# Performance work log

Measured on AMD Instinct MI355X. Metric: run time of the kernel, lower is better.

Reference implementation:

```python
import jax, jax.numpy as jnp
import numpy as np

N, E = 100000, 1600000
F_IN, H, HG, L, C = 128, 128, 128, 3, 40


def setup_inputs() -> dict:
    key = jax.random.key(0)
    ks = jax.random.split(key, 12)
    s = 0.05
    return dict(
        x=jax.random.normal(ks[0], (N, F_IN), jnp.float32),
        edge_index=jax.random.randint(ks[1], (2, E), 0, N),
        edge_weight=jax.random.uniform(ks[2], (E,), jnp.float32),
        h0=jax.random.normal(ks[3], (N, HG), jnp.float32),
        linW=jax.random.normal(ks[4], (F_IN, H), jnp.float32) * s,
        linB=jnp.zeros((H,), jnp.float32),
        convW=jax.random.normal(ks[5], (L, H, H), jnp.float32) * s,
        convB=jnp.zeros((L, H), jnp.float32),
        gru_Wih=jax.random.normal(ks[6], (3 * HG, H), jnp.float32) * s,
        gru_Whh=jax.random.normal(ks[7], (3 * HG, HG), jnp.float32) * s,
        gru_bih=jnp.zeros((3 * HG,), jnp.float32),
        gru_bhh=jnp.zeros((3 * HG,), jnp.float32),
        fcW=jax.random.normal(ks[8], (HG, C), jnp.float32) * s,
        fcB=jnp.zeros((C,), jnp.float32),
    )


def _gru(x, h, Wih, Whh, bih, bhh):
    # torch.nn.GRUCell math (gate order: r, z, n)
    gi = x @ Wih.T + bih  # [N, 3*HG]
    gh = h @ Whh.T + bhh  # [N, 3*HG]
    ir, iz, in_ = jnp.split(gi, 3, axis=-1)
    hr, hz, hn = jnp.split(gh, 3, axis=-1)
    r = jax.nn.sigmoid(ir + hr)
    z = jax.nn.sigmoid(iz + hz)
    n = jnp.tanh(in_ + r * hn)
    return (1.0 - z) * n + z * h


def _gcn_conv(x, src, dst, ew, W, b, n_nodes):
    # PyG GCNConv: linear -> symmetric-normalized sparse aggregation -> bias
    xw = x @ W  # [N, H]
    deg = jax.ops.segment_sum(ew, dst, num_segments=n_nodes)
    dinv = jnp.where(deg > 0, jax.lax.rsqrt(deg), 0.0)
    norm = dinv[src] * ew * dinv[dst]  # [E+N]
    msg = xw[src] * norm[:, None]      # gather + scale (irregular access)
    out = jax.ops.segment_sum(msg, dst, num_segments=n_nodes)  # scatter-add
    return out + b


def reference(x, edge_index, edge_weight, h0, linW, linB, convW, convB,
              gru_Wih, gru_Whh, gru_bih, gru_bhh, fcW, fcB):
    n_nodes = x.shape[0]
    # GCNConv default: add self-loops with weight 1 before normalization
    loops = jnp.arange(n_nodes)
    src = jnp.concatenate([edge_index[0], loops])
    dst = jnp.concatenate([edge_index[1], loops])
    ew = jnp.concatenate([edge_weight, jnp.ones((n_nodes,), edge_weight.dtype)])

    h = h0
    xh = jax.nn.relu(x @ linW + linB)
    h = _gru(xh, h, gru_Wih, gru_Whh, gru_bih, gru_bhh)
    for l in range(convW.shape[0]):  # fixed small layer count
        xh = jax.nn.relu(_gcn_conv(xh, src, dst, ew, convW[l], convB[l], n_nodes))
        h = _gru(xh, h, gru_Wih, gru_Whh, gru_bih, gru_bhh)
    return h @ fcW + fcB
```

## Files before the change

### kernel.cpp

```cpp
#include <hip/hip_runtime.h>
#include <hip/hip_bf16.h>
#include <math.h>

typedef __attribute__((ext_vector_type(8))) short bf8_t;
typedef __attribute__((ext_vector_type(4))) float f4_t;
typedef __attribute__((ext_vector_type(8))) unsigned short us8_t;

__device__ inline unsigned short f2bf(float f) {
  union { float f; unsigned u; } x; x.f = f;
  unsigned r = x.u + 0x7FFF + ((x.u >> 16) & 1);
  return (unsigned short)(r >> 16);
}
__device__ inline float bflo(unsigned v) {
  union { unsigned u; float f; } x; x.u = v << 16; return x.f;
}
__device__ inline float bfhi(unsigned v) {
  union { unsigned u; float f; } x; x.u = v & 0xFFFF0000u; return x.f;
}
__device__ inline float fast_sig(float x) {
  return __builtin_amdgcn_rcpf(1.f + __expf(-x));
}
__device__ inline float fast_tanh(float x) {
  return 1.f - 2.f * __builtin_amdgcn_rcpf(1.f + __expf(2.f * x));
}

__device__ inline void async_copy16(const void* g, void* l) {
  __builtin_amdgcn_global_load_lds(
      (const __attribute__((address_space(1))) unsigned int*)g,
      (__attribute__((address_space(3))) unsigned int*)l, 16, 0, 0);
}

__device__ inline bf8_t pack_bf8(const float* p) {
  float4 a = *(const float4*)p;
  float4 b = *(const float4*)(p + 4);
  bf8_t t;
  t[0] = (short)f2bf(a.x); t[1] = (short)f2bf(a.y);
  t[2] = (short)f2bf(a.z); t[3] = (short)f2bf(a.w);
  t[4] = (short)f2bf(b.x); t[5] = (short)f2bf(b.y);
  t[6] = (short)f2bf(b.z); t[7] = (short)f2bf(b.w);
  return t;
}


__device__ inline void packB_body(const float* __restrict__ W,
                                  unsigned short* __restrict__ out,
                                  int K, int Ncols, int ldw, int trans, int bid) {
  int idx = bid * 256 + threadIdx.x;
  int total = (Ncols / 16) * (K / 32) * 64;
  if (idx >= total) return;
  int lane = idx & 63;
  int frag = idx >> 6;
  int kt = K / 32;
  int k0 = frag % kt;
  int n0 = frag / kt;
  int n = n0 * 16 + (lane & 15);
  int kbase = k0 * 32 + (lane >> 4) * 8;
  us8_t v;
#pragma unroll
  for (int j = 0; j < 8; ++j) {
    int k = kbase + j;
    float f = trans ? W[(size_t)n * ldw + k] : W[(size_t)k * ldw + n];
    v[j] = f2bf(f);
  }
  *(us8_t*)(out + (size_t)idx * 8) = v;
}

template<bool RELU, bool BIAS, bool F32A>
__device__ inline void gemm_body4(const void* __restrict__ Araw,
                                  const unsigned short* __restrict__ Bp,
                                  const float* __restrict__ bias,
                                  unsigned short* __restrict__ C, int M, int bid,
                                  unsigned char* smem) {
  int wave = threadIdx.x >> 6, lane = threadIdx.x & 63;
  int row0 = (bid * 4 + wave) * 16;
  int m = lane & 15, q = lane >> 4;

#pragma unroll
  for (int i = 0; i < 8; ++i) {
    int f = wave * 8 + i;
    async_copy16((const unsigned char*)Bp + (size_t)f * 1024 + lane * 16,
                 smem + f * 1024);
  }
  __syncthreads();
  if (row0 >= M) return;

  int arow = row0 + m; if (arow >= M) arow = M - 1;
  bf8_t a[4];
#pragma unroll
  for (int k0 = 0; k0 < 4; ++k0) {
    if (F32A) {
      a[k0] = pack_bf8((const float*)Araw + (size_t)arow * 128 + k0 * 32 + q * 8);
    } else {
      a[k0] = *(const bf8_t*)((const unsigned short*)Araw +
                              (size_t)arow * 128 + k0 * 32 + q * 8);
    }
  }

#pragma unroll
  for (int n0 = 0; n0 < 8; ++n0) {
    f4_t acc = {};
#pragma unroll
    for (int k0 = 0; k0 < 4; ++k0) {
      bf8_t b = *(const bf8_t*)(smem + (n0 * 4 + k0) * 1024 + lane * 16);
      acc = __builtin_amdgcn_mfma_f32_16x16x32_bf16(a[k0], b, acc, 0, 0, 0);
    }
    int col = n0 * 16 + m;
    float bs = BIAS ? bias[col] : 0.f;
#pragma unroll
    for (int r = 0; r < 4; ++r) {
      int grow = row0 + q * 4 + r;
      if (grow < M) {
        float v = acc[r] + bs;
        if (RELU) v = fmaxf(v, 0.f);
        C[(size_t)grow * 128 + col] = f2bf(v);
      }
    }
  }
}

__device__ inline void gru_stage4(const unsigned short* __restrict__ Bi,
                                  const unsigned short* __restrict__ Bh,
                                  unsigned char* half, int wave, int lane, int g) {
#pragma unroll
  for (int s = 0; s < 6; ++s) {
    int cc = g + 8 * (s >= 3 ? s - 3 : s);
    const unsigned short* src = (s < 3) ? Bi : Bh;
    int f = s * 4 + wave;
    async_copy16((const unsigned char*)src + ((size_t)(cc * 4 + wave)) * 1024 + lane * 16,
                 half + f * 1024);
  }
}

__device__ inline void gru_core4(const bf8_t* ax, const float* h_in, float* h_out,
                                 const unsigned short* __restrict__ Bi,
                                 const unsigned short* __restrict__ Bh,
                                 const float* __restrict__ bih, const float* __restrict__ bhh,
                                 int M, int row0, int wave, int lane,
                                 unsigned char* smem) {
  int m = lane & 15, q = lane >> 4;
  int arow = row0 + m; if (arow >= M) arow = M - 1;

  bf8_t ah[4];
#pragma unroll
  for (int k0 = 0; k0 < 4; ++k0)
    ah[k0] = pack_bf8(h_in + (size_t)arow * 128 + k0 * 32 + q * 8);

  int erow[4];
#pragma unroll
  for (int r = 0; r < 4; ++r) {
    int gr = row0 + q * 4 + r;
    erow[r] = (gr < M) ? gr : (M - 1);
  }

  float hp_cur[4], hp_nxt[4];
#pragma unroll
  for (int r = 0; r < 4; ++r)
    hp_cur[r] = h_in[(size_t)erow[r] * 128 + m];

#pragma unroll
  for (int g = 0; g < 8; ++g) {
    __syncthreads();
    if (g < 7)
      gru_stage4(Bi, Bh, smem + ((g + 1) & 1) * (24 * 1024), wave, lane, g + 1);
    unsigned char* cur = smem + (g & 1) * (24 * 1024);

    f4_t air = {}, aiz = {}, ain = {}, ahr = {}, ahz = {}, ahn = {};
#pragma unroll
    for (int k0 = 0; k0 < 4; ++k0) {
      bf8_t br = *(const bf8_t*)(cur + (0 * 4 + k0) * 1024 + lane * 16);
      bf8_t bz = *(const bf8_t*)(cur + (1 * 4 + k0) * 1024 + lane * 16);
      bf8_t bn = *(const bf8_t*)(cur + (2 * 4 + k0) * 1024 + lane * 16);
      bf8_t cr = *(const bf8_t*)(cur + (3 * 4 + k0) * 1024 + lane * 16);
      bf8_t cz = *(const bf8_t*)(cur + (4 * 4 + k0) * 1024 + lane * 16);
      bf8_t cn = *(const bf8_t*)(cur + (5 * 4 + k0) * 1024 + lane * 16);
      air = __builtin_amdgcn_mfma_f32_16x16x32_bf16(ax[k0], br, air, 0, 0, 0);
      aiz = __builtin_amdgcn_mfma_f32_16x16x32_bf16(ax[k0], bz, aiz, 0, 0, 0);
      ain = __builtin_amdgcn_mfma_f32_16x16x32_bf16(ax[k0], bn, ain, 0, 0, 0);
      ahr = __builtin_amdgcn_mfma_f32_16x16x32_bf16(ah[k0], cr, ahr, 0, 0, 0);
      ahz = __builtin_amdgcn_mfma_f32_16x16x32_bf16(ah[k0], cz, ahz, 0, 0, 0);
      ahn = __builtin_amdgcn_mfma_f32_16x16x32_bf16(ah[k0], cn, ahn, 0, 0, 0);
    }
    if (g < 7) {
#pragma unroll
      for (int r = 0; r < 4; ++r)
        hp_nxt[r] = h_in[(size_t)erow[r] * 128 + (g + 1) * 16 + m];
    }

    int col = g * 16 + m;
    float bir_ = bih[col], biz_ = bih[col + 128], bin_ = bih[col + 256];
    float bhr_ = bhh[col], bhz_ = bhh[col + 128], bhn_ = bhh[col + 256];
#pragma unroll
    for (int r = 0; r < 4; ++r) {
      int grow = row0 + q * 4 + r;
      if (grow < M) {
        float rr = fast_sig(air[r] + bir_ + ahr[r] + bhr_);
        float zz = fast_sig(aiz[r] + biz_ + ahz[r] + bhz_);
        float nn = fast_tanh(ain[r] + bin_ + rr * (ahn[r] + bhn_));
        h_out[(size_t)grow * 128 + col] = (1.f - zz) * nn + zz * hp_cur[r];
      }
    }
#pragma unroll
    for (int r = 0; r < 4; ++r) hp_cur[r] = hp_nxt[r];
  }
}


__global__ __launch_bounds__(256) void k_prep(
    const float* __restrict__ linW, const float* __restrict__ convW,
    const float* __restrict__ Wih, const float* __restrict__ Whh,
    unsigned short* __restrict__ linWp, unsigned short* __restrict__ convWp,
    unsigned short* __restrict__ Bi, unsigned short* __restrict__ Bh,
    int* __restrict__ cnt, int N) {
  int b = blockIdx.x;
  if (b < 8)  { packB_body(linW, linWp, 128, 128, 128, 0, b); return; }
  if (b < 32) { int l = (b - 8) >> 3;
                packB_body(convW + (size_t)l * 16384, convWp + (size_t)l * 16384,
                           128, 128, 128, 0, (b - 8) & 7); return; }
  if (b < 56) { packB_body(Wih, Bi, 128, 384, 128, 1, b - 32); return; }
  if (b < 80) { packB_body(Whh, Bh, 128, 384, 128, 1, b - 56); return; }
  int i = (b - 80) * 256 + threadIdx.x;
  if (i < N) cnt[i] = 0;
}

__global__ __launch_bounds__(256) void k_count_lin(
    const int* __restrict__ dst, int* __restrict__ cnt, int* __restrict__ pos, int E,
    const float* __restrict__ x, const unsigned short* __restrict__ linWp,
    const float* __restrict__ linB, unsigned short* __restrict__ xh, int M,
    int nCnt) {
  __shared__ unsigned char smem[32 * 1024];
  if ((int)blockIdx.x < nCnt) {
    int e = blockIdx.x * 256 + threadIdx.x;
    if (e < E) pos[e] = atomicAdd(&cnt[dst[e]], 1);
    return;
  }
  gemm_body4<true, true, true>(x, linWp, linB, xh, M, blockIdx.x - nCnt, smem);
}

__global__ __launch_bounds__(256) void k_scan_block(
    const int* __restrict__ cnt, int* __restrict__ partial,
    int* __restrict__ bsum, int n) {
  __shared__ int s[256];
  int tid = threadIdx.x;
  int i = blockIdx.x * 256 + tid;
  s[tid] = (i < n) ? cnt[i] : 0;
  __syncthreads();
#pragma unroll
  for (int d = 1; d < 256; d <<= 1) {
    int t = (tid >= d) ? s[tid - d] : 0;
    __syncthreads();
    s[tid] += t;
    __syncthreads();
  }
  if (i < n) partial[i] = s[tid];
  if (tid == 255) bsum[blockIdx.x] = s[255];
}

__global__ __launch_bounds__(512) void k_scan_sums(int* __restrict__ bsum, int nb) {
  __shared__ int s[512];
  int tid = threadIdx.x;
  s[tid] = (tid < nb) ? bsum[tid] : 0;
  __syncthreads();
#pragma unroll
  for (int d = 1; d < 512; d <<= 1) {
    int t = (tid >= d) ? s[tid - d] : 0;
    __syncthreads();
    s[tid] += t;
    __syncthreads();
  }
  if (tid < nb) bsum[tid] = s[tid];
}

__global__ __launch_bounds__(256) void k_scan_add(
    const int* __restrict__ partial, const int* __restrict__ bsum,
    int* __restrict__ rowptr, int n) {
  int i = blockIdx.x * 256 + threadIdx.x;
  if (i == 0) rowptr[0] = 0;
  if (i < n) {
    int v = partial[i] + (blockIdx.x > 0 ? bsum[blockIdx.x - 1] : 0);
    rowptr[i + 1] = v;
  }
}

__global__ __launch_bounds__(512) void k_fill(
    const int* __restrict__ src, const int* __restrict__ dst,
    const float* __restrict__ ew, const int* __restrict__ rowptr,
    const int* __restrict__ pos, int2* __restrict__ csr, int E) {
  int e = blockIdx.x * 512 + threadIdx.x;
  if (e >= E) return;
  int d = dst[e];
  int p = rowptr[d] + pos[e];
  unsigned long long v = (unsigned long long)(unsigned)src[e] |
                         ((unsigned long long)(unsigned)__float_as_int(ew[e]) << 32);
  __builtin_nontemporal_store(v, (unsigned long long*)(csr + p));
}

__global__ __launch_bounds__(512) void k_deg(
    const int* __restrict__ rowptr, const int2* __restrict__ csr,
    float* __restrict__ dinv, int N) {
  int n = blockIdx.x * 512 + threadIdx.x;
  if (n >= N) return;
  int b = rowptr[n], e = rowptr[n + 1];
  float s = 1.0f;
  for (int j = b; j < e; ++j) {
    unsigned long long v = __builtin_nontemporal_load((const unsigned long long*)(csr + j));
    s += __int_as_float((int)(v >> 32));
  }
  dinv[n] = rsqrtf(s);
}

__global__ __launch_bounds__(512) void k_norm(
    const int* __restrict__ rowptr, int2* __restrict__ csr,
    const float* __restrict__ dinv, int N) {
  int n = blockIdx.x * 512 + threadIdx.x;
  if (n >= N) return;
  int b = rowptr[n], e = rowptr[n + 1];
  float dn = dinv[n];
  for (int j = b; j < e; ++j) {
    unsigned long long v = __builtin_nontemporal_load((const unsigned long long*)(csr + j));
    int s = (int)v;
    float w = dinv[s] * __int_as_float((int)(v >> 32)) * dn;
    unsigned long long nv = (unsigned long long)(unsigned)s |
                            ((unsigned long long)(unsigned)__float_as_int(w) << 32);
    __builtin_nontemporal_store(nv, (unsigned long long*)(csr + j));
  }
}

__global__ __launch_bounds__(256) void k_conv(
    const unsigned short* __restrict__ A, const unsigned short* __restrict__ Bp,
    unsigned short* __restrict__ C, int M) {
  __shared__ unsigned char smem[32 * 1024];
  gemm_body4<false, false, false>(A, Bp, nullptr, C, M, blockIdx.x, smem);
}

__global__ __launch_bounds__(256, 3) void k_gru(
    const unsigned short* __restrict__ xh, const float* h_in, float* h_out,
    const unsigned short* __restrict__ Bi, const unsigned short* __restrict__ Bh,
    const float* __restrict__ bih, const float* __restrict__ bhh, int M) {
  __shared__ unsigned char smem[2 * 24 * 1024];
  int wave = threadIdx.x >> 6, lane = threadIdx.x & 63;
  int row0 = (blockIdx.x * 4 + wave) * 16;
  gru_stage4(Bi, Bh, smem, wave, lane, 0);
  int m = lane & 15, q = lane >> 4;
  int arow = row0 + m; if (arow >= M) arow = M - 1;
  bf8_t ax[4];
#pragma unroll
  for (int k0 = 0; k0 < 4; ++k0)
    ax[k0] = *(const bf8_t*)(xh + (size_t)arow * 128 + k0 * 32 + q * 8);
  gru_core4(ax, h_in, h_out, Bi, Bh, bih, bhh, M, row0, wave, lane, smem);
}


__global__ __launch_bounds__(256) void k_gather(
    const int* __restrict__ rowptr, const int2* __restrict__ csr,
    const unsigned* __restrict__ xw,
    const float* __restrict__ dinv, const float* __restrict__ bias,
    unsigned* __restrict__ out, int N) {
  int wave = threadIdx.x >> 6;
  int lane = threadIdx.x & 63;
  int node = __builtin_amdgcn_readfirstlane(blockIdx.x * 4 + wave);
  if (node >= N) return;
  int beg = __builtin_amdgcn_readfirstlane(rowptr[node]);
  int end = __builtin_amdgcn_readfirstlane(rowptr[node + 1]);

  float accl = 0.f, acch = 0.f;
  int k = beg;
  for (; k + 4 <= end; k += 4) {
    unsigned long long r0 = __builtin_nontemporal_load((const unsigned long long*)(csr + k));
    unsigned long long r1 = __builtin_nontemporal_load((const unsigned long long*)(csr + k + 1));
    unsigned long long r2 = __builtin_nontemporal_load((const unsigned long long*)(csr + k + 2));
    unsigned long long r3 = __builtin_nontemporal_load((const unsigned long long*)(csr + k + 3));
    unsigned v0 = xw[((size_t)(unsigned)r0 << 6) + lane];
    unsigned v1 = xw[((size_t)(unsigned)r1 << 6) + lane];
    unsigned v2 = xw[((size_t)(unsigned)r2 << 6) + lane];
    unsigned v3 = xw[((size_t)(unsigned)r3 << 6) + lane];
    float w0 = __int_as_float((int)(r0 >> 32)), w1 = __int_as_float((int)(r1 >> 32));
    float w2 = __int_as_float((int)(r2 >> 32)), w3 = __int_as_float((int)(r3 >> 32));
    accl += bflo(v0) * w0; acch += bfhi(v0) * w0;
    accl += bflo(v1) * w1; acch += bfhi(v1) * w1;
    accl += bflo(v2) * w2; acch += bfhi(v2) * w2;
    accl += bflo(v3) * w3; acch += bfhi(v3) * w3;
  }
  for (; k < end; ++k) {
    unsigned long long r = __builtin_nontemporal_load((const unsigned long long*)(csr + k));
    unsigned v = xw[((size_t)(unsigned)r << 6) + lane];
    float w = __int_as_float((int)(r >> 32));
    accl += bflo(v) * w; acch += bfhi(v) * w;
  }

  float di = dinv[node];
  float sn = di * di;
  unsigned vs = xw[((size_t)node << 6) + lane];
  float2 b = *(const float2*)(bias + lane * 2);
  float rl = fmaxf(accl + bflo(vs) * sn + b.x, 0.f);
  float rh = fmaxf(acch + bfhi(vs) * sn + b.y, 0.f);
  unsigned o = (unsigned)f2bf(rl) | ((unsigned)f2bf(rh) << 16);
  out[((size_t)node << 6) + lane] = o;
}


template<bool RELU, bool BIAS>
__global__ __launch_bounds__(256) void k_gemm128(
    const float* __restrict__ A, const float* __restrict__ B,
    const float* __restrict__ bias, float* __restrict__ C, int M, int Nc) {
  __shared__ float As[64][36];
  __shared__ float Bs[32][64];
  int tid = threadIdx.x;
  int tx = tid & 15, ty = tid >> 4;
  int row0 = blockIdx.y * 64, col0 = blockIdx.x * 64;
  float acc[4][4] = {};

  for (int k0 = 0; k0 < 128; k0 += 32) {
#pragma unroll
    for (int i = 0; i < 2; ++i) {
      int f = tid + i * 256;
      int r = f >> 3, c4 = f & 7;
      int gr = row0 + r;
      float4 v = make_float4(0.f, 0.f, 0.f, 0.f);
      if (gr < M) v = *(const float4*)(A + (size_t)gr * 128 + k0 + c4 * 4);
      *(float4*)(&As[r][c4 * 4]) = v;
    }
#pragma unroll
    for (int i = 0; i < 2; ++i) {
      int f = tid + i * 256;
      int r = f >> 4, c4 = f & 15;
      int gc = col0 + c4 * 4;
      float4 v = make_float4(0.f, 0.f, 0.f, 0.f);
      if (gc + 3 < Nc) v = *(const float4*)(B + (size_t)(k0 + r) * Nc + gc);
      *(float4*)(&Bs[r][c4 * 4]) = v;
    }
    __syncthreads();
#pragma unroll
    for (int kk = 0; kk < 32; ++kk) {
      float4 b = *(float4*)(&Bs[kk][tx * 4]);
      float a0 = As[ty * 4 + 0][kk];
      float a1 = As[ty * 4 + 1][kk];
      float a2 = As[ty * 4 + 2][kk];
      float a3 = As[ty * 4 + 3][kk];
      acc[0][0] += a0 * b.x; acc[0][1] += a0 * b.y; acc[0][2] += a0 * b.z; acc[0][3] += a0 * b.w;
      acc[1][0] += a1 * b.x; acc[1][1] += a1 * b.y; acc[1][2] += a1 * b.z; acc[1][3] += a1 * b.w;
      acc[2][0] += a2 * b.x; acc[2][1] += a2 * b.y; acc[2][2] += a2 * b.z; acc[2][3] += a2 * b.w;
      acc[3][0] += a3 * b.x; acc[3][1] += a3 * b.y; acc[3][2] += a3 * b.z; acc[3][3] += a3 * b.w;
    }
    __syncthreads();
  }

#pragma unroll
  for (int i = 0; i < 4; ++i) {
    int gr = row0 + ty * 4 + i;
    if (gr >= M) continue;
#pragma unroll
    for (int j = 0; j < 4; ++j) {
      int gc = col0 + tx * 4 + j;
      if (gc >= Nc) continue;
      float v = acc[i][j];
      if (BIAS) v += bias[gc];
      if (RELU) v = fmaxf(v, 0.f);
      C[(size_t)gr * Nc + gc] = v;
    }
  }
}


extern "C" void kernel_launch(void* const* d_in, const int* in_sizes, int n_in,
                              void* d_out, int out_size, void* d_ws, size_t ws_size,
                              hipStream_t stream) {
  const float* x    = (const float*)d_in[0];
  const int*   ei   = (const int*)d_in[1];
  const float* ew   = (const float*)d_in[2];
  const float* h0   = (const float*)d_in[3];
  const float* linW = (const float*)d_in[4];
  const float* linB = (const float*)d_in[5];
  const float* convW= (const float*)d_in[6];
  const float* convB= (const float*)d_in[7];
  const float* Wih  = (const float*)d_in[8];
  const float* Whh  = (const float*)d_in[9];
  const float* bih  = (const float*)d_in[10];
  const float* bhh  = (const float*)d_in[11];
  const float* fcW  = (const float*)d_in[12];
  const float* fcB  = (const float*)d_in[13];

  int N = in_sizes[0] / 128;
  int E = in_sizes[1] / 2;
  const int* srcI = ei;
  const int* dstI = ei + E;
  int nb = (N + 255) / 256;

  float* ws = (float*)d_ws;
  size_t off = 0;
  float* dinv = ws + off; off += (size_t)N;
  if (off & 1) off++;
  float* h    = ws + off; off += (size_t)N * 128;
  int* iws = (int*)(ws + off);
  size_t ioff = 0;
  int2* csr    = (int2*)iws; ioff += (size_t)2 * E;
  int* cnt     = iws + ioff; ioff += (size_t)N;
  int* partial = iws + ioff; ioff += (size_t)N;
  int* bsum    = iws + ioff; ioff += 512;
  int* rowptr  = iws + ioff; ioff += (size_t)N + 1;
  ioff = (ioff + 3) & ~(size_t)3;
  unsigned short* usws = (unsigned short*)(iws + ioff);
  size_t uoff = 0;
  unsigned short* xh_bf  = usws + uoff; uoff += (size_t)N * 128;
  unsigned short* xw_bf  = usws + uoff; uoff += (size_t)N * 128;
  unsigned short* linWp  = usws + uoff; uoff += 128 * 128;
  unsigned short* convWp = usws + uoff; uoff += 3 * 128 * 128;
  unsigned short* Bi     = usws + uoff; uoff += 384 * 128;
  unsigned short* Bh     = usws + uoff; uoff += 384 * 128;

  int* pos = (int*)xw_bf;

  int gw4  = (N + 63) / 64;
  int nCnt = (E + 255) / 256;
  int n512 = (N + 511) / 512;
  int e512 = (E + 511) / 512;
  int ggat = (N + 3) / 4;

  k_prep<<<80 + nb, 256, 0, stream>>>(linW, convW, Wih, Whh,
                                      linWp, convWp, Bi, Bh, cnt, N);
  k_count_lin<<<nCnt + gw4, 256, 0, stream>>>(dstI, cnt, pos, E,
                                              x, linWp, linB, xh_bf, N, nCnt);
  k_scan_block<<<nb, 256, 0, stream>>>(cnt, partial, bsum, N);
  k_scan_sums<<<1, 512, 0, stream>>>(bsum, nb);
  k_scan_add<<<nb, 256, 0, stream>>>(partial, bsum, rowptr, N);
  k_fill<<<e512, 512, 0, stream>>>(srcI, dstI, ew, rowptr, pos, csr, E);
  k_deg<<<n512, 512, 0, stream>>>(rowptr, csr, dinv, N);
  k_norm<<<n512, 512, 0, stream>>>(rowptr, csr, dinv, N);
  k_gru<<<gw4, 256, 0, stream>>>(xh_bf, h0, h, Bi, Bh, bih, bhh, N);
  for (int l = 0; l < 3; ++l) {
    k_conv<<<gw4, 256, 0, stream>>>(
        xh_bf, convWp + (size_t)l * 128 * 128, xw_bf, N);
    k_gather<<<ggat, 256, 0, stream>>>(
        rowptr, csr, (const unsigned*)xw_bf, dinv, convB + (size_t)l * 128,
        (unsigned*)xh_bf, N);
    k_gru<<<gw4, 256, 0, stream>>>(xh_bf, h, h, Bi, Bh, bih, bhh, N);
  }
  dim3 g40(1, (N + 63) / 64);
  k_gemm128<false, true><<<g40, 256, 0, stream>>>(h, fcW, fcB, (float*)d_out, N, 40);
}
```

Before: 888.2 us.

## Co-schedule independent kernels via block-partitioned launches and unroll gather by 8

Merges independent stages into single launches by splitting the grid: the CSR fill runs alongside the first GRU, the degree computation alongside the first conv GEMM, and each later GRU alongside the next layer's conv GEMM, since both only read xh. This cuts launch count and lets small memory-bound work overlap with compute-bound GEMM blocks. The gather loop also gains an 8-way unrolled path to keep more loads in flight. The cost is that fused kernels take the larger shared-memory footprint and launch bounds, which may lower occupancy for the lighter block type.

```diff
diff --git a/kernel.cpp b/kernel.cpp
--- a/kernel.cpp
+++ b/kernel.cpp
@@ -65,6 +65,40 @@
   *(us8_t*)(out + (size_t)idx * 8) = v;
 }
 
+__device__ inline void fill_body(const int* __restrict__ src, const int* __restrict__ dst,
+                                 const float* __restrict__ ew, const int* __restrict__ rowptr,
+                                 const int* __restrict__ pos, int2* __restrict__ csr,
+                                 int E, int bid) {
+#pragma unroll
+  for (int t = 0; t < 2; ++t) {
+    int e = bid * 512 + t * 256 + threadIdx.x;
+    if (e < E) {
+      int d = dst[e];
+      int p = rowptr[d] + pos[e];
+      unsigned long long v = (unsigned long long)(unsigned)src[e] |
+                             ((unsigned long long)(unsigned)__float_as_int(ew[e]) << 32);
+      __builtin_nontemporal_store(v, (unsigned long long*)(csr + p));
+    }
+  }
+}
+
+__device__ inline void deg_body(const int* __restrict__ rowptr, const int2* __restrict__ csr,
+                                float* __restrict__ dinv, int N, int bid) {
+#pragma unroll
+  for (int t = 0; t < 2; ++t) {
+    int n = bid * 512 + t * 256 + threadIdx.x;
+    if (n < N) {
+      int b = rowptr[n], e = rowptr[n + 1];
+      float s = 1.0f;
+      for (int j = b; j < e; ++j) {
+        unsigned long long v = __builtin_nontemporal_load((const unsigned long long*)(csr + j));
+        s += __int_as_float((int)(v >> 32));
+      }
+      dinv[n] = rsqrtf(s);
+    }
+  }
+}
+
 template<bool RELU, bool BIAS, bool F32A>
 __device__ inline void gemm_body4(const void* __restrict__ Araw,
                                   const unsigned short* __restrict__ Bp,
@@ -202,6 +236,24 @@
 #pragma unroll
     for (int r = 0; r < 4; ++r) hp_cur[r] = hp_nxt[r];
   }
+}
+
+__device__ inline void gru_body4(const unsigned short* __restrict__ xh,
+                                 const float* h_in, float* h_out,
+                                 const unsigned short* __restrict__ Bi,
+                                 const unsigned short* __restrict__ Bh,
+                                 const float* __restrict__ bih, const float* __restrict__ bhh,
+                                 int M, int bid, unsigned char* smem) {
+  int wave = threadIdx.x >> 6, lane = threadIdx.x & 63;
+  int row0 = (bid * 4 + wave) * 16;
+  gru_stage4(Bi, Bh, smem, wave, lane, 0);
+  int m = lane & 15, q = lane >> 4;
+  int arow = row0 + m; if (arow >= M) arow = M - 1;
+  bf8_t ax[4];
+#pragma unroll
+  for (int k0 = 0; k0 < 4; ++k0)
+    ax[k0] = *(const bf8_t*)(xh + (size_t)arow * 128 + k0 * 32 + q * 8);
+  gru_core4(ax, h_in, h_out, Bi, Bh, bih, bhh, M, row0, wave, lane, smem);
 }
 
 
@@ -281,31 +333,32 @@
   }
 }
 
-__global__ __launch_bounds__(512) void k_fill(
-    const int* __restrict__ src, const int* __restrict__ dst,
+__global__ __launch_bounds__(256, 3) void k_fill_gru(
+    const unsigned short* __restrict__ xh, const float* h_in, float* h_out,
+    const unsigned short* __restrict__ Bi, const unsigned short* __restrict__ Bh,
+    const float* __restrict__ bih, const float* __restrict__ bhh, int M,
+    const int* __restrict__ src, const int* __restrict__ dstI,
     const float* __restrict__ ew, const int* __restrict__ rowptr,
-    const int* __restrict__ pos, int2* __restrict__ csr, int E) {
-  int e = blockIdx.x * 512 + threadIdx.x;
-  if (e >= E) return;
-  int d = dst[e];
-  int p = rowptr[d] + pos[e];
-  unsigned long long v = (unsigned long long)(unsigned)src[e] |
-                         ((unsigned long long)(unsigned)__float_as_int(ew[e]) << 32);
-  __builtin_nontemporal_store(v, (unsigned long long*)(csr + p));
-}
-
-__global__ __launch_bounds__(512) void k_deg(
+    const int* __restrict__ pos, int2* __restrict__ csr, int E, int nGru) {
+  __shared__ unsigned char smem[2 * 24 * 1024];
+  if ((int)blockIdx.x < nGru) {
+    gru_body4(xh, h_in, h_out, Bi, Bh, bih, bhh, M, blockIdx.x, smem);
+    return;
+  }
+  fill_body(src, dstI, ew, rowptr, pos, csr, E, blockIdx.x - nGru);
+}
+
+__global__ __launch_bounds__(256) void k_deg_conv(
+    const unsigned short* __restrict__ A, const unsigned short* __restrict__ Bp,
+    unsigned short* __restrict__ C, int M,
     const int* __restrict__ rowptr, const int2* __restrict__ csr,
-    float* __restrict__ dinv, int N) {
-  int n = blockIdx.x * 512 + threadIdx.x;
-  if (n >= N) return;
-  int b = rowptr[n], e = rowptr[n + 1];
-  float s = 1.0f;
-  for (int j = b; j < e; ++j) {
-    unsigned long long v = __builtin_nontemporal_load((const unsigned long long*)(csr + j));
-    s += __int_as_float((int)(v >> 32));
-  }
-  dinv[n] = rsqrtf(s);
+    float* __restrict__ dinv, int N, int nConv) {
+  __shared__ unsigned char smem[32 * 1024];
+  if ((int)blockIdx.x < nConv) {
+    gemm_body4<false, false, false>(A, Bp, nullptr, C, M, blockIdx.x, smem);
+    return;
+  }
+  deg_body(rowptr, csr, dinv, N, blockIdx.x - nConv);
 }
 
 __global__ __launch_bounds__(512) void k_norm(
@@ -325,11 +378,18 @@
   }
 }
 
-__global__ __launch_bounds__(256) void k_conv(
-    const unsigned short* __restrict__ A, const unsigned short* __restrict__ Bp,
-    unsigned short* __restrict__ C, int M) {
-  __shared__ unsigned char smem[32 * 1024];
-  gemm_body4<false, false, false>(A, Bp, nullptr, C, M, blockIdx.x, smem);
+__global__ __launch_bounds__(256, 3) void k_gru_conv(
+    const unsigned short* __restrict__ xh, const float* h_in, float* h_out,
+    const unsigned short* __restrict__ Bi, const unsigned short* __restrict__ Bh,
+    const float* __restrict__ bih, const float* __restrict__ bhh,
+    const unsigned short* __restrict__ Bp, unsigned short* __restrict__ xw,
+    int M, int nGru) {
+  __shared__ unsigned char smem[2 * 24 * 1024];
+  if ((int)blockIdx.x < nGru) {
+    gru_body4(xh, h_in, h_out, Bi, Bh, bih, bhh, M, blockIdx.x, smem);
+    return;
+  }
+  gemm_body4<false, false, false>(xh, Bp, nullptr, xw, M, blockIdx.x - nGru, smem);
 }
 
 __global__ __launch_bounds__(256, 3) void k_gru(
@@ -337,16 +397,7 @@
     const unsigned short* __restrict__ Bi, const unsigned short* __restrict__ Bh,
     const float* __restrict__ bih, const float* __restrict__ bhh, int M) {
   __shared__ unsigned char smem[2 * 24 * 1024];
-  int wave = threadIdx.x >> 6, lane = threadIdx.x & 63;
-  int row0 = (blockIdx.x * 4 + wave) * 16;
-  gru_stage4(Bi, Bh, smem, wave, lane, 0);
-  int m = lane & 15, q = lane >> 4;
-  int arow = row0 + m; if (arow >= M) arow = M - 1;
-  bf8_t ax[4];
-#pragma unroll
-  for (int k0 = 0; k0 < 4; ++k0)
-    ax[k0] = *(const bf8_t*)(xh + (size_t)arow * 128 + k0 * 32 + q * 8);
-  gru_core4(ax, h_in, h_out, Bi, Bh, bih, bhh, M, row0, wave, lane, smem);
+  gru_body4(xh, h_in, h_out, Bi, Bh, bih, bhh, M, blockIdx.x, smem);
 }
 
 
@@ -364,6 +415,36 @@
 
   float accl = 0.f, acch = 0.f;
   int k = beg;
+  for (; k + 8 <= end; k += 8) {
+    unsigned long long r0 = __builtin_nontemporal_load((const unsigned long long*)(csr + k));
+    unsigned long long r1 = __builtin_nontemporal_load((const unsigned long long*)(csr + k + 1));
+    unsigned long long r2 = __builtin_nontemporal_load((const unsigned long long*)(csr + k + 2));
+    unsigned long long r3 = __builtin_nontemporal_load((const unsigned long long*)(csr + k + 3));
+    unsigned long long r4 = __builtin_nontemporal_load((const unsigned long long*)(csr + k + 4));
+    unsigned long long r5 = __builtin_nontemporal_load((const unsigned long long*)(csr + k + 5));
+    unsigned long long r6 = __builtin_nontemporal_load((const unsigned long long*)(csr + k + 6));
+    unsigned long long r7 = __builtin_nontemporal_load((const unsigned long long*)(csr + k + 7));
+    unsigned v0 = xw[((size_t)(unsigned)r0 << 6) + lane];
+    unsigned v1 = xw[((size_t)(unsigned)r1 << 6) + lane];
+    unsigned v2 = xw[((size_t)(unsigned)r2 << 6) + lane];
+    unsigned v3 = xw[((size_t)(unsigned)r3 << 6) + lane];
+    unsigned v4 = xw[((size_t)(unsigned)r4 << 6) + lane];
+    unsigned v5 = xw[((size_t)(unsigned)r5 << 6) + lane];
+    unsigned v6 = xw[((size_t)(unsigned)r6 << 6) + lane];
+    unsigned v7 = xw[((size_t)(unsigned)r7 << 6) + lane];
+    float w0 = __int_as_float((int)(r0 >> 32)), w1 = __int_as_float((int)(r1 >> 32));
+    float w2 = __int_as_float((int)(r2 >> 32)), w3 = __int_as_float((int)(r3 >> 32));
+    float w4 = __int_as_float((int)(r4 >> 32)), w5 = __int_as_float((int)(r5 >> 32));
+    float w6 = __int_as_float((int)(r6 >> 32)), w7 = __int_as_float((int)(r7 >> 32));
+    accl += bflo(v0) * w0; acch += bfhi(v0) * w0;
+    accl += bflo(v1) * w1; acch += bfhi(v1) * w1;
+    accl += bflo(v2) * w2; acch += bfhi(v2) * w2;
+    accl += bflo(v3) * w3; acch += bfhi(v3) * w3;
+    accl += bflo(v4) * w4; acch += bfhi(v4) * w4;
+    accl += bflo(v5) * w5; acch += bfhi(v5) * w5;
+    accl += bflo(v6) * w6; acch += bfhi(v6) * w6;
+    accl += bflo(v7) * w7; acch += bfhi(v7) * w7;
+  }
   for (; k + 4 <= end; k += 4) {
     unsigned long long r0 = __builtin_nontemporal_load((const unsigned long long*)(csr + k));
     unsigned long long r1 = __builtin_nontemporal_load((const unsigned long long*)(csr + k + 1));
@@ -522,17 +603,23 @@
   k_scan_block<<<nb, 256, 0, stream>>>(cnt, partial, bsum, N);
   k_scan_sums<<<1, 512, 0, stream>>>(bsum, nb);
   k_scan_add<<<nb, 256, 0, stream>>>(partial, bsum, rowptr, N);
-  k_fill<<<e512, 512, 0, stream>>>(srcI, dstI, ew, rowptr, pos, csr, E);
-  k_deg<<<n512, 512, 0, stream>>>(rowptr, csr, dinv, N);
+  k_fill_gru<<<gw4 + e512, 256, 0, stream>>>(
+      xh_bf, h0, h, Bi, Bh, bih, bhh, N,
+      srcI, dstI, ew, rowptr, pos, csr, E, gw4);
+  k_deg_conv<<<gw4 + n512, 256, 0, stream>>>(
+      xh_bf, convWp, xw_bf, N, rowptr, csr, dinv, N, gw4);
   k_norm<<<n512, 512, 0, stream>>>(rowptr, csr, dinv, N);
-  k_gru<<<gw4, 256, 0, stream>>>(xh_bf, h0, h, Bi, Bh, bih, bhh, N);
   for (int l = 0; l < 3; ++l) {
-    k_conv<<<gw4, 256, 0, stream>>>(
-        xh_bf, convWp + (size_t)l * 128 * 128, xw_bf, N);
     k_gather<<<ggat, 256, 0, stream>>>(
         rowptr, csr, (const unsigned*)xw_bf, dinv, convB + (size_t)l * 128,
         (unsigned*)xh_bf, N);
-    k_gru<<<gw4, 256, 0, stream>>>(xh_bf, h, h, Bi, Bh, bih, bhh, N);
+    if (l < 2) {
+      k_gru_conv<<<2 * gw4, 256, 0, stream>>>(
+          xh_bf, h, h, Bi, Bh, bih, bhh,
+          convWp + (size_t)(l + 1) * 128 * 128, xw_bf, N, gw4);
+    } else {
+      k_gru<<<gw4, 256, 0, stream>>>(xh_bf, h, h, Bi, Bh, bih, bhh, N);
+    }
   }
   dim3 g40(1, (N + 63) / 64);
   k_gemm128<false, true><<<g40, 256, 0, stream>>>(h, fcW, fcB, (float*)d_out, N, 40);
```

Result: slower. 1.034 ms (+16.4%).

## Drop edge-normalization pass and fuse block-sum scan into scan-add

Applied to the files above, without the earlier changes.

Removes the k_norm kernel that rewrote every CSR entry with the symmetric normalization weight, and instead computes dinv[src]*ew*dinv[dst] on the fly inside each gather. It also folds the single-block scan of block sums into k_scan_add, so every block redundantly scans the sums in shared memory. This saves one full read/write pass over the edge list and two launches. The cost is an extra random dinv load and two multiplies per edge in each of the three gather layers.

```diff
diff --git a/kernel.cpp b/kernel.cpp
--- a/kernel.cpp
+++ b/kernel.cpp
@@ -255,30 +255,27 @@
   if (tid == 255) bsum[blockIdx.x] = s[255];
 }
 
-__global__ __launch_bounds__(512) void k_scan_sums(int* __restrict__ bsum, int nb) {
+__global__ __launch_bounds__(256) void k_scan_add(
+    const int* __restrict__ partial, const int* __restrict__ bsum,
+    int* __restrict__ rowptr, int n, int nb) {
   __shared__ int s[512];
   int tid = threadIdx.x;
   s[tid] = (tid < nb) ? bsum[tid] : 0;
+  s[tid + 256] = (tid + 256 < nb) ? bsum[tid + 256] : 0;
   __syncthreads();
 #pragma unroll
   for (int d = 1; d < 512; d <<= 1) {
-    int t = (tid >= d) ? s[tid - d] : 0;
-    __syncthreads();
-    s[tid] += t;
-    __syncthreads();
-  }
-  if (tid < nb) bsum[tid] = s[tid];
-}
-
-__global__ __launch_bounds__(256) void k_scan_add(
-    const int* __restrict__ partial, const int* __restrict__ bsum,
-    int* __restrict__ rowptr, int n) {
-  int i = blockIdx.x * 256 + threadIdx.x;
+    int t0 = (tid >= d) ? s[tid - d] : 0;
+    int t1 = (tid + 256 >= d) ? s[tid + 256 - d] : 0;
+    __syncthreads();
+    s[tid] += t0;
+    s[tid + 256] += t1;
+    __syncthreads();
+  }
+  int base = (blockIdx.x > 0) ? s[blockIdx.x - 1] : 0;
+  int i = blockIdx.x * 256 + tid;
   if (i == 0) rowptr[0] = 0;
-  if (i < n) {
-    int v = partial[i] + (blockIdx.x > 0 ? bsum[blockIdx.x - 1] : 0);
-    rowptr[i + 1] = v;
-  }
+  if (i < n) rowptr[i + 1] = partial[i] + base;
 }
 
 __global__ __launch_bounds__(512) void k_fill(
@@ -308,23 +305,6 @@
   dinv[n] = rsqrtf(s);
 }
 
-__global__ __launch_bounds__(512) void k_norm(
-    const int* __restrict__ rowptr, int2* __restrict__ csr,
-    const float* __restrict__ dinv, int N) {
-  int n = blockIdx.x * 512 + threadIdx.x;
-  if (n >= N) return;
-  int b = rowptr[n], e = rowptr[n + 1];
-  float dn = dinv[n];
-  for (int j = b; j < e; ++j) {
-    unsigned long long v = __builtin_nontemporal_load((const unsigned long long*)(csr + j));
-    int s = (int)v;
-    float w = dinv[s] * __int_as_float((int)(v >> 32)) * dn;
-    unsigned long long nv = (unsigned long long)(unsigned)s |
-                            ((unsigned long long)(unsigned)__float_as_int(w) << 32);
-    __builtin_nontemporal_store(nv, (unsigned long long*)(csr + j));
-  }
-}
-
 __global__ __launch_bounds__(256) void k_conv(
     const unsigned short* __restrict__ A, const unsigned short* __restrict__ Bp,
     unsigned short* __restrict__ C, int M) {
@@ -361,6 +341,7 @@
   if (node >= N) return;
   int beg = __builtin_amdgcn_readfirstlane(rowptr[node]);
   int end = __builtin_amdgcn_readfirstlane(rowptr[node + 1]);
+  float di = dinv[node];
 
   float accl = 0.f, acch = 0.f;
   int k = beg;
@@ -373,8 +354,10 @@
     unsigned v1 = xw[((size_t)(unsigned)r1 << 6) + lane];
     unsigned v2 = xw[((size_t)(unsigned)r2 << 6) + lane];
     unsigned v3 = xw[((size_t)(unsigned)r3 << 6) + lane];
-    float w0 = __int_as_float((int)(r0 >> 32)), w1 = __int_as_float((int)(r1 >> 32));
-    float w2 = __int_as_float((int)(r2 >> 32)), w3 = __int_as_float((int)(r3 >> 32));
+    float w0 = dinv[(unsigned)r0] * __int_as_float((int)(r0 >> 32)) * di;
+    float w1 = dinv[(unsigned)r1] * __int_as_float((int)(r1 >> 32)) * di;
+    float w2 = dinv[(unsigned)r2] * __int_as_float((int)(r2 >> 32)) * di;
+    float w3 = dinv[(unsigned)r3] * __int_as_float((int)(r3 >> 32)) * di;
     accl += bflo(v0) * w0; acch += bfhi(v0) * w0;
     accl += bflo(v1) * w1; acch += bfhi(v1) * w1;
     accl += bflo(v2) * w2; acch += bfhi(v2) * w2;
@@ -383,11 +366,10 @@
   for (; k < end; ++k) {
     unsigned long long r = __builtin_nontemporal_load((const unsigned long long*)(csr + k));
     unsigned v = xw[((size_t)(unsigned)r << 6) + lane];
-    float w = __int_as_float((int)(r >> 32));
+    float w = dinv[(unsigned)r] * __int_as_float((int)(r >> 32)) * di;
     accl += bflo(v) * w; acch += bfhi(v) * w;
   }
 
-  float di = dinv[node];
   float sn = di * di;
   unsigned vs = xw[((size_t)node << 6) + lane];
   float2 b = *(const float2*)(bias + lane * 2);
@@ -520,11 +502,9 @@
   k_count_lin<<<nCnt + gw4, 256, 0, stream>>>(dstI, cnt, pos, E,
                                               x, linWp, linB, xh_bf, N, nCnt);
   k_scan_block<<<nb, 256, 0, stream>>>(cnt, partial, bsum, N);
-  k_scan_sums<<<1, 512, 0, stream>>>(bsum, nb);
-  k_scan_add<<<nb, 256, 0, stream>>>(partial, bsum, rowptr, N);
+  k_scan_add<<<nb, 256, 0, stream>>>(partial, bsum, rowptr, N, nb);
   k_fill<<<e512, 512, 0, stream>>>(srcI, dstI, ew, rowptr, pos, csr, E);
   k_deg<<<n512, 512, 0, stream>>>(rowptr, csr, dinv, N);
-  k_norm<<<n512, 512, 0, stream>>>(rowptr, csr, dinv, N);
   k_gru<<<gw4, 256, 0, stream>>>(xh_bf, h0, h, Bi, Bh, bih, bhh, N);
   for (int l = 0; l < 3; ++l) {
     k_conv<<<gw4, 256, 0, stream>>>(
```

Measured after the change: 868.5 us. 1.02x faster.
